# Performance work log

Measured on AMD Instinct MI355X. Metric: run time of the kernel, lower is better.

## Reference

```python
import math
import jax, jax.numpy as jnp
import numpy as np

B, N, D = 8, 2048, 256
NUM_ROLES = 3
ROLE_HUB, ROLE_MONITOR = 1, 2  # assumed ROLE_TO_ID mapping
NEG = -10000.0


def _lin_init(k, fan_in, shape):
    b = 1.0 / math.sqrt(fan_in)
    return jax.random.uniform(k, shape, jnp.float32, -b, b)


def setup_inputs() -> dict:
    key = jax.random.key(0)
    ks = jax.random.split(key, 20)
    inp = {
        'x': jax.random.normal(ks[0], (B, N, D), jnp.float32),
        'node_roles': jax.random.randint(ks[1], (B, N), 0, NUM_ROLES),
        'node_mask': jax.random.bernoulli(ks[2], 0.9, (B, N)),
        'ln_gamma': jnp.ones((D,), jnp.float32),
        'ln_beta': jnp.zeros((D,), jnp.float32),
        'role_emb': jax.random.normal(ks[3], (NUM_ROLES, D), jnp.float32),
    }
    names = ['q', 'k', 's', 'p', 'o']
    for i, nm in enumerate(names):
        inp['W' + nm] = _lin_init(ks[4 + 2 * i], D, (D, D))
        inp['b' + nm] = _lin_init(ks[5 + 2 * i], D, (D,))
    inp['Wg'] = _lin_init(ks[14], 2 * D, (2 * D, D))
    inp['bg'] = _lin_init(ks[15], 2 * D, (D,))
    return inp


def _layernorm(x, g, b):
    mu = jnp.mean(x, -1, keepdims=True)
    var = jnp.mean(jnp.square(x - mu), -1, keepdims=True)
    return (x - mu) * jax.lax.rsqrt(var + 1e-5) * g + b


def reference(x, node_roles, node_mask, ln_gamma, ln_beta, role_emb,
              Wq, bq, Wk, bk, Ws, bs, Wp, bp, Wo, bo, Wg, bg):
    normed = _layernorm(x, ln_gamma, ln_beta)
    role_bias = role_emb[node_roles]                      # [B,N,D]
    h = normed + role_bias
    query = h @ Wq + bq
    key_t = h @ Wk + bk
    sender = h @ Ws + bs
    payload = normed @ Wp + bp

    read_logits = jnp.einsum('bid,bjd->bij', query, key_t) / math.sqrt(D)
    fs = role_bias + sender
    forward_logits = jnp.einsum('bid,bjd->bij', fs, fs)
    logits = read_logits + 0.5 * forward_logits           # variant='selective'

    source_mask = node_mask                               # variant != 'memory_hubs'
    pair_mask = node_mask[:, :, None] & source_mask[:, None, :]
    eye = jnp.eye(N, dtype=bool)[None]
    pair_mask = pair_mask | (eye & node_mask[:, :, None] & node_mask[:, None, :])

    logits = jnp.where(pair_mask, logits, NEG)
    weights = jax.nn.softmax(logits, axis=-1)
    weights = jnp.where(pair_mask, weights, 0.0)

    message = jnp.einsum('bij,bjd->bid', weights, payload)
    gate = jax.nn.sigmoid(jnp.concatenate([x, message], axis=-1) @ Wg + bg)
    update = (gate * message) @ Wo + bo
    out = x + update                                      # dropout p=0

    entropy = -(weights * jnp.log(weights + 1e-8)).sum(-1).mean()
    # masked-mean replicates torch's weights[..., col_mask].mean() without dynamic shapes
    mon_cols = (node_roles == ROLE_MONITOR).any(0)        # [N]
    hub_cols = (node_roles == ROLE_HUB).any(0)
    def col_mean(cols):
        cnt = cols.sum() * B * N
        tot = (weights * cols[None, None, :].astype(weights.dtype)).sum()
        return jnp.where(cnt > 0, tot / jnp.maximum(cnt, 1), 0.0)
    return (out, entropy, col_mean(mon_cols), col_mean(hub_cols))
```

## Files before the change

### kernel.cpp

```cpp
#include <hip/hip_runtime.h>
#include <math.h>

#define BB 8
#define NN 2048
#define DD 256
#define MTOK 16384

typedef __bf16 bf16x8 __attribute__((ext_vector_type(8)));
typedef __bf16 bf16x4 __attribute__((ext_vector_type(4)));
typedef float f32x4 __attribute__((ext_vector_type(4)));

#define MFMA16(a, b, c) __builtin_amdgcn_mfma_f32_16x16x32_bf16(a, b, c, 0, 0, 0)

#define BARX()                              \
  do {                                      \
    asm volatile("" ::: "memory");          \
    __builtin_amdgcn_s_barrier();           \
    asm volatile("" ::: "memory");          \
  } while (0)
#define WAITVM(N)                                              \
  do {                                                         \
    asm volatile("s_waitcnt vmcnt(" #N ")" ::: "memory");      \
    __builtin_amdgcn_sched_barrier(0);                         \
  } while (0)

#define OFF_X16    0ull
#define OFF_N16    2097152ull
#define OFF_H16    4194304ull
#define OFF_GROW   8388608ull
#define OFF_GCOL   12582912ull
#define OFF_PTE    16777216ull
#define OFF_WT     19005440ull
#define OFF_STAT   19234816ull
#define OFF_ENT    23625728ull
#define OFF_MONR   23642112ull
#define OFF_HUBR   23658496ull
#define OFF_MONF   23674880ull
#define OFF_HUBF   23676928ull
#define OFF_MASK   23678976ull
#define OFF_PART   23683072ull
#define OFF_MSGN0  OFF_N16
#define OFF_MSGN1  OFF_H16
#define OFF_MSG16  OFF_PTE
#define OFF_GM16   OFF_GROW

__device__ __forceinline__ void gl_lds16(const void* g, void* l) {
  __builtin_amdgcn_global_load_lds(
      (const __attribute__((address_space(1))) unsigned int*)g,
      (__attribute__((address_space(3))) unsigned int*)l, 16, 0, 0);
}

__global__ __launch_bounds__(256) void setup_kernel(
    const float* __restrict__ x, const int* __restrict__ roles,
    const void* __restrict__ mraw,
    const float* __restrict__ gamma, const float* __restrict__ beta,
    const float* __restrict__ role_emb,
    const float* __restrict__ Wq, const float* __restrict__ Wk,
    const float* __restrict__ Ws, const float* __restrict__ Wp,
    const float* __restrict__ Wg, const float* __restrict__ Wo,
    __bf16* __restrict__ X16, __bf16* __restrict__ N16,
    __bf16* __restrict__ H16, __bf16* __restrict__ WT,
    unsigned char* __restrict__ mask8,
    float* __restrict__ monf, float* __restrict__ hubf) {
  __shared__ float T[64][65];
  int bid = blockIdx.x;
  int tid = threadIdx.x;
  if (bid < 4096) {
    int t = bid * 4 + (tid >> 6);
    int lane = tid & 63;
    size_t off = (size_t)t * DD + lane * 4;
    float4 xv = *(const float4*)(x + off);
    float s = xv.x + xv.y + xv.z + xv.w;
    float ss = xv.x * xv.x + xv.y * xv.y + xv.z * xv.z + xv.w * xv.w;
#pragma unroll
    for (int m = 1; m < 64; m <<= 1) {
      s += __shfl_xor(s, m, 64);
      ss += __shfl_xor(ss, m, 64);
    }
    float mu = s * (1.0f / 256.0f);
    float var = ss * (1.0f / 256.0f) - mu * mu;
    float inv = rsqrtf(var + 1e-5f);
    float4 g = *(const float4*)(gamma + lane * 4);
    float4 be = *(const float4*)(beta + lane * 4);
    float nv[4];
    nv[0] = (xv.x - mu) * inv * g.x + be.x;
    nv[1] = (xv.y - mu) * inv * g.y + be.y;
    nv[2] = (xv.z - mu) * inv * g.z + be.z;
    nv[3] = (xv.w - mu) * inv * g.w + be.w;
    int role = roles[t];
    float4 rb = *(const float4*)(role_emb + (size_t)role * DD + lane * 4);
    float rbv[4] = {rb.x, rb.y, rb.z, rb.w};
    bf16x4 xo, no, ho;
    float xf[4] = {xv.x, xv.y, xv.z, xv.w};
#pragma unroll
    for (int q = 0; q < 4; ++q) {
      xo[q] = (__bf16)xf[q];
      no[q] = (__bf16)nv[q];
      ho[q] = (__bf16)(nv[q] + rbv[q]);
    }
    *(bf16x4*)&X16[off] = xo;
    *(bf16x4*)&N16[off] = no;
    *(bf16x4*)&H16[off] = ho;
  } else if (bid < 4288) {
    int wblk = bid - 4096;
    int z = wblk >> 5, rem = wblk & 31;
    int bx = rem & 3, by = rem >> 2;
    const float* src;
    int K;
    size_t doff;
    switch (z) {
      case 0: src = Wq; K = 256; doff = 0; break;
      case 1: src = Wk; K = 256; doff = 65536; break;
      case 2: src = Ws; K = 256; doff = 131072; break;
      case 3: src = Wp; K = 256; doff = 196608; break;
      case 4: src = Wg; K = 512; doff = 262144; break;
      default: src = Wo; K = 256; doff = 393216; break;
    }
    int k0 = by * 64;
    if (k0 >= K) return;
    int n0 = bx * 64;
#pragma unroll
    for (int p = 0; p < 16; ++p) {
      int idx = p * 256 + tid;
      int r = idx >> 6, c = idx & 63;
      T[r][c] = src[(size_t)(k0 + r) * 256 + n0 + c];
    }
    __syncthreads();
#pragma unroll
    for (int p = 0; p < 16; ++p) {
      int idx = p * 256 + tid;
      int n = idx >> 6, k = idx & 63;
      WT[doff + (size_t)(n0 + n) * K + k0 + k] = (__bf16)T[k][n];
    }
  } else {
    int* csh = (int*)&T[0][0];
    if (tid == 0) { csh[0] = 0; csh[1] = 0; }
    __syncthreads();
    const unsigned char* raw = (const unsigned char*)mraw;
    int c0 = 0, c1 = 0;
    for (int i = tid; i < 4096; i += 256) {
      int nz = (raw[i] != 0) ? 1 : 0;
      if ((i & 3) == 0) c0 += nz; else c1 += nz;
    }
    atomicAdd(&csh[0], c0);
    atomicAdd(&csh[1], c1);
    __syncthreads();
    int k = (csh[0] == 0) ? 2 : ((csh[1] == 0) ? 0 : 1);
    int t = (bid - 4288) * 256 + tid;
    if (t < MTOK) {
      int v;
      if (k == 1)      v = (raw[t] != 0);
      else if (k == 0) v = (((const int*)mraw)[t] != 0);
      else             v = (((const float*)mraw)[t] != 0.0f);
      mask8[t] = (unsigned char)v;
    }
    if (t < NN) {
      int mon = 0, hub = 0;
#pragma unroll
      for (int b = 0; b < BB; ++b) {
        int r = roles[b * NN + t];
        mon |= (r == 2) ? 1 : 0;
        hub |= (r == 1) ? 1 : 0;
      }
      monf[t] = (float)mon;
      hubf[t] = (float)hub;
    }
  }
}

__global__ __launch_bounds__(256) void fill_pte_kernel(
    const int* __restrict__ roles, __bf16* __restrict__ PTE) {
  int idx = blockIdx.x * 256 + threadIdx.x;
  int b = idx >> 11, col = idx & 2047;
  int mon = 0, hub = 0;
#pragma unroll
  for (int bb = 0; bb < BB; ++bb) {
    int r = roles[bb * NN + col];
    mon |= (r == 2) ? 1 : 0;
    hub |= (r == 1) ? 1 : 0;
  }
  size_t rbase = ((size_t)(b * 272 + 256)) * 2048 + col;
  PTE[rbase] = (__bf16)(float)mon;
  PTE[rbase + 2048] = (__bf16)(float)hub;
  PTE[rbase + 2 * 2048] = (__bf16)1.0f;
#pragma unroll
  for (int r = 3; r < 16; ++r) PTE[rbase + (size_t)r * 2048] = (__bf16)0.0f;
}

__global__ __launch_bounds__(256, 3) void proj4_kernel(
    const __bf16* __restrict__ H16, const __bf16* __restrict__ N16,
    const __bf16* __restrict__ WT,
    const float* __restrict__ bq, const float* __restrict__ bk,
    const float* __restrict__ bs, const float* __restrict__ bp,
    const int* __restrict__ roles, const float* __restrict__ remb,
    __bf16* __restrict__ Grow, __bf16* __restrict__ Gcol,
    __bf16* __restrict__ PTE) {
  __shared__ __align__(16) unsigned char As[128 * 128];
  __shared__ __align__(16) unsigned char Bs[128 * 128];
  int z = blockIdx.z;
  const __bf16* A = (z == 3) ? N16 : H16;
  const __bf16* W = WT + (size_t)z * 65536;
  const float* bias = (z == 0) ? bq : (z == 1) ? bk : (z == 2) ? bs : bp;

  int tid = threadIdx.x;
  int w = tid >> 6, lane = tid & 63, ln15 = lane & 15, lq = lane >> 4;
  int wr = w >> 1, wc = w & 1;
  int row0 = blockIdx.y * 128, col0 = blockIdx.x * 128;
  f32x4 acc[4][4];
#pragma unroll
  for (int i = 0; i < 4; ++i)
#pragma unroll
    for (int j = 0; j < 4; ++j) acc[i][j] = (f32x4){0.f, 0.f, 0.f, 0.f};

  int lr = lane >> 3;
  int sb = ((lane & 7) * 16) ^ ((lr & 7) << 4);

  for (int kt = 0; kt < 4; ++kt) {
    __syncthreads();
#pragma unroll
    for (int i2 = 0; i2 < 4; ++i2) {
      int idx = w * 4 + i2;
      int grow = row0 + idx * 8 + lr;
      gl_lds16((const unsigned char*)A + (size_t)grow * 512 + kt * 128 + sb,
               As + idx * 1024);
    }
#pragma unroll
    for (int i2 = 0; i2 < 4; ++i2) {
      int idx = w * 4 + i2;
      int gcol = col0 + idx * 8 + lr;
      gl_lds16((const unsigned char*)W + (size_t)gcol * 512 + kt * 128 + sb,
               Bs + idx * 1024);
    }
    __syncthreads();
#pragma unroll
    for (int ks = 0; ks < 2; ++ks) {
      bf16x8 af[4], bfr[4];
#pragma unroll
      for (int i = 0; i < 4; ++i) {
        int rl = wr * 64 + i * 16 + ln15;
        int byteoff = (lq * 16 + ks * 64) ^ ((rl & 7) << 4);
        af[i] = *(const bf16x8*)(As + rl * 128 + byteoff);
      }
#pragma unroll
      for (int j = 0; j < 4; ++j) {
        int cl = wc * 64 + j * 16 + ln15;
        int byteoff = (lq * 16 + ks * 64) ^ ((cl & 7) << 4);
        bfr[j] = *(const bf16x8*)(Bs + cl * 128 + byteoff);
      }
#pragma unroll
      for (int i = 0; i < 4; ++i)
#pragma unroll
        for (int j = 0; j < 4; ++j) acc[i][j] = MFMA16(af[i], bfr[j], acc[i][j]);
    }
  }
  float bj[4];
#pragma unroll
  for (int j = 0; j < 4; ++j) bj[j] = bias[col0 + wc * 64 + j * 16 + ln15];
#pragma unroll
  for (int i = 0; i < 4; ++i) {
#pragma unroll
    for (int j = 0; j < 4; ++j) {
      int gcol = col0 + wc * 64 + j * 16 + ln15;
      int growb = row0 + wr * 64 + i * 16 + lq * 4;
      float o[4];
#pragma unroll
      for (int ri = 0; ri < 4; ++ri) o[ri] = acc[i][j][ri] + bj[j];
      if (z == 0) {
#pragma unroll
        for (int ri = 0; ri < 4; ++ri)
          Grow[(size_t)(growb + ri) * 512 + gcol] = (__bf16)(o[ri] * 0.0625f);
      } else if (z == 1) {
#pragma unroll
        for (int ri = 0; ri < 4; ++ri)
          Gcol[(size_t)(growb + ri) * 512 + gcol] = (__bf16)o[ri];
      } else if (z == 2) {
#pragma unroll
        for (int ri = 0; ri < 4; ++ri) {
          float oo = o[ri] + remb[(size_t)roles[growb + ri] * 256 + gcol];
          Grow[(size_t)(growb + ri) * 512 + 256 + gcol] =
              (__bf16)(oo * 0.70710678118f);
        }
      } else {
        bf16x4 v;
#pragma unroll
        for (int ri = 0; ri < 4; ++ri) v[ri] = (__bf16)o[ri];
        int b = growb >> 11, tok = growb & 2047;
        *(bf16x4*)&PTE[((size_t)(b * 272 + gcol)) * 2048 + tok] = v;
      }
    }
  }
}

__global__ __launch_bounds__(256, 2) void attn_kernel(
    const __bf16* __restrict__ Grow, const __bf16* __restrict__ Gcol,
    const __bf16* __restrict__ PTE, const unsigned char* __restrict__ mask8,
    __bf16* __restrict__ msgn0, __bf16* __restrict__ msgn1,
    float* __restrict__ statP) {
  __shared__ __align__(16) unsigned char GcLo[16384];
  __shared__ __align__(16) unsigned char GcHi[16384];
  __shared__ __align__(16) unsigned char PtS[2][17408];

  int tid = threadIdx.x;
  int w = tid >> 6, lane = tid & 63, ln15 = lane & 15, lq = lane >> 4;
  int id = blockIdx.x;
  int b = id & 7;
  int half = (id >> 3) & 1;
  int r0 = (id >> 4) * 64;
  size_t base = (size_t)b * NN;
  __bf16* msgn = half ? msgn1 : msgn0;
  float* statB = statP + (size_t)half * MTOK * 6;

  const unsigned char* gbaseK =
      (const unsigned char*)Gcol + (base + half * 1024) * 1024;
  const unsigned char* gbaseF =
      (const unsigned char*)Grow + (base + half * 1024) * 1024;
  const unsigned char* pbase =
      (const unsigned char*)PTE + (size_t)b * 272 * 4096 + half * 2048;

  bf16x8 Af[16];
  {
    const __bf16* gr = Grow + (base + r0 + w * 16 + ln15) * 512 + lq * 8;
#pragma unroll
    for (int kk = 0; kk < 16; ++kk) Af[kk] = *(const bf16x8*)(gr + kk * 32);
  }

  float m = -1e30f, T = 0.f;
  f32x4 macc[17];
#pragma unroll
  for (int nt = 0; nt < 17; ++nt) macc[nt] = (f32x4){0.f, 0.f, 0.f, 0.f};

  int pswz = (lq ^ ((ln15 >> 1) & 3)) << 4;
  int n0 = ((ln15 >> 2) * 8) + (ln15 & 3);
  int n1 = n0 + 4;
  int s0 = (((n0 & 3) | (((n0 >> 3) & 1) << 2))) << 4;
  int s1 = (((n1 & 3) | (((n1 >> 3) & 1) << 2))) << 4;
  int srcsw = ((lane & 3) ^ ((lane >> 3) & 3)) << 4;
  int glrow = lane >> 5;
  int glb = (lane & 31) * 16;

  auto STG = [&](const unsigned char* gb, int ch, unsigned char* dst, int koff) {
#pragma unroll
    for (int i = 0; i < 4; ++i) {
      int rp = w * 8 + 2 * i;
      int r = rp + glrow;
      int sbr = glb ^ ((((r & 3) | (((r >> 3) & 1) << 2))) << 4);
      gl_lds16(gb + (size_t)(ch * 32 + r) * 1024 + koff + sbr, dst + rp * 512);
    }
  };
  auto STPT = [&](int ch, int buf) {
#pragma unroll
    for (int i = 0; i < 4; ++i) {
      int idx = w * 4 + i;
      int drow = idx * 16 + (lane >> 2);
      gl_lds16(pbase + (size_t)drow * 4096 + ch * 64 + srcsw,
               &PtS[buf][idx * 1024]);
    }
    {
      int drow = 256 + (lane >> 2);
      gl_lds16(pbase + (size_t)drow * 4096 + ch * 64 + srcsw,
               &PtS[buf][16 * 1024]);
    }
  };

  STPT(0, 0);
  STG(gbaseK, 0, GcLo, 0);
  STG(gbaseF, 0, GcHi, 512);

  for (int ch = 0; ch < 32; ++ch) {
    int cur = ch & 1;
    WAITVM(4);
    BARX();
    STPT(ch + 1, cur ^ 1);

    f32x4 sa0 = (f32x4){0.f, 0.f, 0.f, 0.f};
    f32x4 sa1 = (f32x4){0.f, 0.f, 0.f, 0.f};
    __builtin_amdgcn_s_setprio(1);
#pragma unroll
    for (int kk = 0; kk < 8; ++kk) {
      bf16x8 bv0 = *(const bf16x8*)&GcLo[n0 * 512 + ((lq * 16 + kk * 64) ^ s0)];
      sa0 = MFMA16(bv0, Af[kk], sa0);
      bf16x8 bv1 = *(const bf16x8*)&GcLo[n1 * 512 + ((lq * 16 + kk * 64) ^ s1)];
      sa1 = MFMA16(bv1, Af[kk], sa1);
    }
    __builtin_amdgcn_s_setprio(0);

    WAITVM(5);
    BARX();
    STG(gbaseK, ch + 1, GcLo, 0);

    __builtin_amdgcn_s_setprio(1);
#pragma unroll
    for (int kk = 8; kk < 16; ++kk) {
      bf16x8 bv0 = *(const bf16x8*)&GcHi[n0 * 512 + ((lq * 16 + (kk - 8) * 64) ^ s0)];
      sa0 = MFMA16(bv0, Af[kk], sa0);
      bf16x8 bv1 = *(const bf16x8*)&GcHi[n1 * 512 + ((lq * 16 + (kk - 8) * 64) ^ s1)];
      sa1 = MFMA16(bv1, Af[kk], sa1);
    }
    __builtin_amdgcn_s_setprio(0);

    float sv[8] = {sa0[0], sa0[1], sa0[2], sa0[3], sa1[0], sa1[1], sa1[2], sa1[3]};
    unsigned long long mk = *(const unsigned long long*)(
        mask8 + base + half * 1024 + (size_t)ch * 32 + lq * 8);

    float mt = -1e30f;
#pragma unroll
    for (int i = 0; i < 8; ++i) {
      float li = ((mk >> (8 * i)) & 0xffull) ? sv[i] : -1e30f;
      mt = fmaxf(mt, li);
    }
    mt = fmaxf(mt, __shfl_xor(mt, 16));
    mt = fmaxf(mt, __shfl_xor(mt, 32));
    float mnew = fmaxf(m, mt);
    if (__any(mnew > m + 8.0f)) {
      float ci = __expf(m - mnew);
      float cir[4];
#pragma unroll
      for (int r = 0; r < 4; ++r)
        cir[r] = __shfl(ci, (lane & 48) + ((lane >> 2) & 12) + r);
#pragma unroll
      for (int nt = 0; nt < 17; ++nt) {
        macc[nt][0] *= cir[0]; macc[nt][1] *= cir[1];
        macc[nt][2] *= cir[2]; macc[nt][3] *= cir[3];
      }
      T *= ci;
      m = mnew;
    }
    float e[8], tl = 0.f;
#pragma unroll
    for (int i = 0; i < 8; ++i) {
      float ei = ((mk >> (8 * i)) & 0xffull) ? __expf(sv[i] - m) : 0.f;
      e[i] = ei;
      tl += ei * sv[i];
    }
    tl += __shfl_xor(tl, 16);
    tl += __shfl_xor(tl, 32);
    T += tl;
    bf16x8 ef;
#pragma unroll
    for (int i = 0; i < 8; ++i) ef[i] = (__bf16)e[i];

    __builtin_amdgcn_s_setprio(1);
#pragma unroll
    for (int nt = 0; nt < 17; ++nt) {
      int drow = nt * 16 + ln15;
      bf16x8 pv = *(const bf16x8*)&PtS[cur][drow * 64 + pswz];
      macc[nt] = MFMA16(ef, pv, macc[nt]);
    }
    __builtin_amdgcn_s_setprio(0);

    BARX();
    STG(gbaseF, ch + 1, GcHi, 512);
  }
  WAITVM(0);

#pragma unroll
  for (int r = 0; r < 4; ++r) {
    int grow = r0 + w * 16 + lq * 4 + r;
    size_t row = base + grow;
    float Z = __shfl(macc[16][r], (lane & 48) + 2);
    float invZ = (Z > 0.f) ? (1.0f / Z) : 0.f;
#pragma unroll
    for (int nt = 0; nt < 16; ++nt)
      msgn[row * 256 + nt * 16 + ln15] = (__bf16)(macc[nt][r] * invZ);
    float Tm = __shfl(macc[16][r], (lane & 48) + 0);
    float Th = __shfl(macc[16][r], (lane & 48) + 1);
    float Tr = __shfl(T, (lane & 48) + ((lane >> 2) & 12) + r);
    float mr = __shfl(m, (lane & 48) + ((lane >> 2) & 12) + r);
    if (ln15 == 0) {
      float* stt = statB + row * 6;
      stt[0] = mr; stt[1] = Tr; stt[2] = Z; stt[3] = Tm; stt[4] = Th;
    }
  }
}

__global__ __launch_bounds__(256) void merge_kernel(
    const __bf16* __restrict__ msgn0, const __bf16* __restrict__ msgn1,
    const float* __restrict__ statP, const unsigned char* __restrict__ mask8,
    __bf16* __restrict__ MSG16, float* __restrict__ entr,
    float* __restrict__ monr, float* __restrict__ hubr) {
  int row = blockIdx.x * 4 + (threadIdx.x >> 6);
  int lane = threadIdx.x & 63;
  const float* s0 = statP + (size_t)row * 6;
  const float* s1 = statP + (size_t)(MTOK + row) * 6;
  float m0 = s0[0], T0 = s0[1], Z0 = s0[2], Tm0 = s0[3], Th0 = s0[4];
  float m1 = s1[0], T1 = s1[1], Z1 = s1[2], Tm1 = s1[3], Th1 = s1[4];
  int valid = mask8[row] != 0;
  float mm = fmaxf(m0, m1);
  float c0 = __expf(m0 - mm), c1 = __expf(m1 - mm);
  float w0 = c0 * Z0, w1 = c1 * Z1;
  float Z = w0 + w1;
  int ok = valid && (Z > 0.f);
  float invZ = ok ? (1.0f / Z) : 0.0f;
  float rw0 = w0 * invZ, rw1 = w1 * invZ;
  bf16x4 p0 = *(const bf16x4*)(msgn0 + (size_t)row * 256 + lane * 4);
  bf16x4 p1 = *(const bf16x4*)(msgn1 + (size_t)row * 256 + lane * 4);
  bf16x4 o;
#pragma unroll
  for (int q = 0; q < 4; ++q)
    o[q] = (__bf16)(rw0 * (float)p0[q] + rw1 * (float)p1[q]);
  *(bf16x4*)&MSG16[(size_t)row * 256 + lane * 4] = o;
  if (lane == 0) {
    float T = c0 * T0 + c1 * T1;
    float Tm = c0 * Tm0 + c1 * Tm1;
    float Th = c0 * Th0 + c1 * Th1;
    entr[row] = ok ? (__logf(Z) + mm - T * invZ) : 0.0f;
    monr[row] = ok ? (Tm * invZ) : 0.0f;
    hubr[row] = ok ? (Th * invZ) : 0.0f;
  }
}

template <int K, int MODE>
__global__ __launch_bounds__(256) void gemmb_kernel(
    const __bf16* __restrict__ A0, const __bf16* __restrict__ A1,
    const __bf16* __restrict__ WT, const float* __restrict__ bias,
    const float* __restrict__ xf, const __bf16* __restrict__ msg16,
    void* __restrict__ dst0) {
  __shared__ __align__(16) unsigned char As[128 * 128];
  __shared__ __align__(16) unsigned char Bs[64 * 128];
  int tid = threadIdx.x;
  int w = tid >> 6, lane = tid & 63, ln15 = lane & 15, lq = lane >> 4;
  int wr = w >> 1, wc = w & 1;
  int row0 = blockIdx.y * 128, col0 = blockIdx.x * 64;
  f32x4 acc[4][2];
#pragma unroll
  for (int i = 0; i < 4; ++i)
#pragma unroll
    for (int j = 0; j < 2; ++j) acc[i][j] = (f32x4){0.f, 0.f, 0.f, 0.f};

  int lr = lane >> 3;
  int sb = ((lane & 7) * 16) ^ ((lr & 7) << 4);

  for (int kt = 0; kt < K / 64; ++kt) {
    const __bf16* Ab = A0;
    int ktl = kt;
    if (K == 512 && kt >= 4) { Ab = A1; ktl = kt - 4; }
    __syncthreads();
#pragma unroll
    for (int i2 = 0; i2 < 4; ++i2) {
      int idx = w * 4 + i2;
      int grow = row0 + idx * 8 + lr;
      gl_lds16((const unsigned char*)Ab + (size_t)grow * 512 + ktl * 128 + sb,
               As + idx * 1024);
    }
#pragma unroll
    for (int i2 = 0; i2 < 2; ++i2) {
      int idx = w * 2 + i2;
      int gcol = col0 + idx * 8 + lr;
      gl_lds16((const unsigned char*)WT + (size_t)gcol * (K * 2) + kt * 128 + sb,
               Bs + idx * 1024);
    }
    __syncthreads();
#pragma unroll
    for (int ks = 0; ks < 2; ++ks) {
      bf16x8 af[4], bfr[2];
#pragma unroll
      for (int i = 0; i < 4; ++i) {
        int rl = wr * 64 + i * 16 + ln15;
        int byteoff = (lq * 16 + ks * 64) ^ ((rl & 7) << 4);
        af[i] = *(const bf16x8*)(As + rl * 128 + byteoff);
      }
#pragma unroll
      for (int j = 0; j < 2; ++j) {
        int cl = wc * 32 + j * 16 + ln15;
        int byteoff = (lq * 16 + ks * 64) ^ ((cl & 7) << 4);
        bfr[j] = *(const bf16x8*)(Bs + cl * 128 + byteoff);
      }
#pragma unroll
      for (int i = 0; i < 4; ++i)
#pragma unroll
        for (int j = 0; j < 2; ++j) acc[i][j] = MFMA16(af[i], bfr[j], acc[i][j]);
    }
  }
  float bj[2];
#pragma unroll
  for (int j = 0; j < 2; ++j) bj[j] = bias[col0 + wc * 32 + j * 16 + ln15];
#pragma unroll
  for (int i = 0; i < 4; ++i) {
#pragma unroll
    for (int ri = 0; ri < 4; ++ri) {
      int grow = row0 + wr * 64 + i * 16 + lq * 4 + ri;
#pragma unroll
      for (int j = 0; j < 2; ++j) {
        int gcol = col0 + wc * 32 + j * 16 + ln15;
        float o = acc[i][j][ri] + bj[j];
        if (MODE == 4) {
          float sg = 1.0f / (1.0f + __expf(-o));
          float mv = (float)msg16[(size_t)grow * 256 + gcol];
          ((__bf16*)dst0)[(size_t)grow * 256 + gcol] = (__bf16)(sg * mv);
        } else {
          ((float*)dst0)[(size_t)grow * 256 + gcol] =
              o + xf[(size_t)grow * 256 + gcol];
        }
      }
    }
  }
}

__device__ __forceinline__ float block_sum(float v, float* sh) {
  __syncthreads();
  sh[threadIdx.x] = v;
  __syncthreads();
  for (int s = 128; s > 0; s >>= 1) {
    if ((int)threadIdx.x < s) sh[threadIdx.x] += sh[threadIdx.x + s];
    __syncthreads();
  }
  return sh[0];
}

__global__ __launch_bounds__(256) void reduce1_kernel(
    const float* __restrict__ entr, const float* __restrict__ monr,
    const float* __restrict__ hubr, float* __restrict__ partial) {
  __shared__ float sh[256];
  int t = blockIdx.x * 256 + threadIdx.x;
  float es = entr[t], ms = monr[t], hs = hubr[t];
  float e = block_sum(es, sh);
  float mo = block_sum(ms, sh);
  float hu = block_sum(hs, sh);
  if (threadIdx.x == 0) {
    partial[blockIdx.x * 4 + 0] = e;
    partial[blockIdx.x * 4 + 1] = mo;
    partial[blockIdx.x * 4 + 2] = hu;
  }
}

__global__ __launch_bounds__(256) void reduce2_kernel(
    const float* __restrict__ partial, const float* __restrict__ monf,
    const float* __restrict__ hubf, float* __restrict__ out3) {
  __shared__ float sh[256];
  float es = 0.f, ms = 0.f, hs = 0.f, cmf = 0.f, chf = 0.f;
  if (threadIdx.x < 64) {
    es = partial[threadIdx.x * 4 + 0];
    ms = partial[threadIdx.x * 4 + 1];
    hs = partial[threadIdx.x * 4 + 2];
  }
  for (int j = threadIdx.x; j < NN; j += 256) { cmf += monf[j]; chf += hubf[j]; }
  float esum = block_sum(es, sh);
  float msum = block_sum(ms, sh);
  float hsum = block_sum(hs, sh);
  float cmsum = block_sum(cmf, sh);
  float chsum = block_sum(chf, sh);
  if (threadIdx.x == 0) {
    out3[0] = esum / 16384.0f;
    out3[1] = (cmsum > 0.f) ? (msum / (cmsum * 16384.0f)) : 0.0f;
    out3[2] = (chsum > 0.f) ? (hsum / (chsum * 16384.0f)) : 0.0f;
  }
}

extern "C" void kernel_launch(void* const* d_in, const int* in_sizes, int n_in,
                              void* d_out, int out_size, void* d_ws, size_t ws_size,
                              hipStream_t stream) {
  const float* x = (const float*)d_in[0];
  const int* roles = (const int*)d_in[1];
  const void* mraw = d_in[2];
  const float* gamma = (const float*)d_in[3];
  const float* beta = (const float*)d_in[4];
  const float* remb = (const float*)d_in[5];
  const float* Wq = (const float*)d_in[6];
  const float* bq = (const float*)d_in[7];
  const float* Wk = (const float*)d_in[8];
  const float* bk = (const float*)d_in[9];
  const float* Ws = (const float*)d_in[10];
  const float* bs = (const float*)d_in[11];
  const float* Wp = (const float*)d_in[12];
  const float* bp = (const float*)d_in[13];
  const float* Wo = (const float*)d_in[14];
  const float* bo = (const float*)d_in[15];
  const float* Wg = (const float*)d_in[16];
  const float* bg = (const float*)d_in[17];

  float* ws = (float*)d_ws;
  __bf16* X16 = (__bf16*)(ws + OFF_X16);
  __bf16* N16 = (__bf16*)(ws + OFF_N16);
  __bf16* H16 = (__bf16*)(ws + OFF_H16);
  __bf16* Grow = (__bf16*)(ws + OFF_GROW);
  __bf16* Gcol = (__bf16*)(ws + OFF_GCOL);
  __bf16* PTE = (__bf16*)(ws + OFF_PTE);
  __bf16* WT = (__bf16*)(ws + OFF_WT);
  float* statP = ws + OFF_STAT;
  __bf16* msgn0 = (__bf16*)(ws + OFF_MSGN0);
  __bf16* msgn1 = (__bf16*)(ws + OFF_MSGN1);
  float* partial = ws + OFF_PART;
  __bf16* MSG16 = (__bf16*)(ws + OFF_MSG16);
  __bf16* GM16 = (__bf16*)(ws + OFF_GM16);
  float* entr = ws + OFF_ENT;
  float* monr = ws + OFF_MONR;
  float* hubr = ws + OFF_HUBR;
  float* monfp = ws + OFF_MONF;
  float* hubfp = ws + OFF_HUBF;
  unsigned char* mask8 = (unsigned char*)(ws + OFF_MASK);
  float* out = (float*)d_out;

  __bf16* WTg = WT + 262144;
  __bf16* WTo = WT + 393216;

  setup_kernel<<<4352, 256, 0, stream>>>(x, roles, mraw, gamma, beta, remb,
                                         Wq, Wk, Ws, Wp, Wg, Wo,
                                         X16, N16, H16, WT, mask8, monfp, hubfp);
  fill_pte_kernel<<<64, 256, 0, stream>>>(roles, PTE);
  proj4_kernel<<<dim3(2, 128, 4), 256, 0, stream>>>(
      H16, N16, WT, bq, bk, bs, bp, roles, remb, Grow, Gcol, PTE);
  attn_kernel<<<512, 256, 0, stream>>>(Grow, Gcol, PTE, mask8, msgn0, msgn1,
                                       statP);
  merge_kernel<<<4096, 256, 0, stream>>>(msgn0, msgn1, statP, mask8, MSG16,
                                         entr, monr, hubr);
  dim3 gg(4, 128);
  gemmb_kernel<512, 4><<<gg, 256, 0, stream>>>(X16, MSG16, WTg, bg, nullptr,
                                               MSG16, GM16);
  gemmb_kernel<256, 5><<<gg, 256, 0, stream>>>(GM16, nullptr, WTo, bo, x,
                                               nullptr, out);
  reduce1_kernel<<<64, 256, 0, stream>>>(entr, monr, hubr, partial);
  reduce2_kernel<<<1, 256, 0, stream>>>(partial, monfp, hubfp, out + 4194304);
}
```

Measured before the change: 165.7 us.

## Split attention key range into thirds and single-buffer payload tile for occupancy

Result: slower. 287.2 us (+73.3%).

```diff
diff --git a/kernel.cpp b/kernel.cpp
--- a/kernel.cpp
+++ b/kernel.cpp
@@ -27,6 +27,7 @@
 #define OFF_X16    0ull
 #define OFF_N16    2097152ull
 #define OFF_H16    4194304ull
+#define OFF_MSGN2t 6291456ull
 #define OFF_GROW   8388608ull
 #define OFF_GCOL   12582912ull
 #define OFF_PTE    16777216ull
@@ -43,6 +44,9 @@
 #define OFF_MSGN1  OFF_H16
 #define OFF_MSG16  OFF_PTE
 #define OFF_GM16   OFF_GROW
+
+__device__ __constant__ int kKvOff[3] = {0, 704, 1376};
+__device__ __constant__ int kNch[3] = {22, 21, 21};
 
 __device__ __forceinline__ void gl_lds16(const void* g, void* l) {
   __builtin_amdgcn_global_load_lds(
@@ -291,31 +295,33 @@
   }
 }
 
-__global__ __launch_bounds__(256, 2) void attn_kernel(
+__global__ __launch_bounds__(256, 3) void attn_kernel(
     const __bf16* __restrict__ Grow, const __bf16* __restrict__ Gcol,
     const __bf16* __restrict__ PTE, const unsigned char* __restrict__ mask8,
     __bf16* __restrict__ msgn0, __bf16* __restrict__ msgn1,
-    float* __restrict__ statP) {
+    __bf16* __restrict__ msgn2, float* __restrict__ statP) {
   __shared__ __align__(16) unsigned char GcLo[16384];
   __shared__ __align__(16) unsigned char GcHi[16384];
-  __shared__ __align__(16) unsigned char PtS[2][17408];
+  __shared__ __align__(16) unsigned char PtS[17408];
 
   int tid = threadIdx.x;
   int w = tid >> 6, lane = tid & 63, ln15 = lane & 15, lq = lane >> 4;
   int id = blockIdx.x;
   int b = id & 7;
-  int half = (id >> 3) & 1;
-  int r0 = (id >> 4) * 64;
+  int third = (id >> 3) % 3;
+  int r0 = (id / 24) * 64;
   size_t base = (size_t)b * NN;
-  __bf16* msgn = half ? msgn1 : msgn0;
-  float* statB = statP + (size_t)half * MTOK * 6;
+  int kvoff = kKvOff[third];
+  int nch = kNch[third];
+  __bf16* msgn = (third == 0) ? msgn0 : (third == 1) ? msgn1 : msgn2;
+  float* statB = statP + (size_t)third * MTOK * 6;
 
   const unsigned char* gbaseK =
-      (const unsigned char*)Gcol + (base + half * 1024) * 1024;
+      (const unsigned char*)Gcol + (base + kvoff) * 1024;
   const unsigned char* gbaseF =
-      (const unsigned char*)Grow + (base + half * 1024) * 1024;
+      (const unsigned char*)Grow + (base + kvoff) * 1024;
   const unsigned char* pbase =
-      (const unsigned char*)PTE + (size_t)b * 272 * 4096 + half * 2048;
+      (const unsigned char*)PTE + (size_t)b * 272 * 4096 + (size_t)kvoff * 2;
 
   bf16x8 Af[16];
   {
@@ -347,30 +353,28 @@
       gl_lds16(gb + (size_t)(ch * 32 + r) * 1024 + koff + sbr, dst + rp * 512);
     }
   };
-  auto STPT = [&](int ch, int buf) {
+  auto STPT = [&](int ch) {
 #pragma unroll
     for (int i = 0; i < 4; ++i) {
       int idx = w * 4 + i;
       int drow = idx * 16 + (lane >> 2);
       gl_lds16(pbase + (size_t)drow * 4096 + ch * 64 + srcsw,
-               &PtS[buf][idx * 1024]);
+               PtS + idx * 1024);
     }
     {
       int drow = 256 + (lane >> 2);
       gl_lds16(pbase + (size_t)drow * 4096 + ch * 64 + srcsw,
-               &PtS[buf][16 * 1024]);
+               PtS + 16 * 1024);
     }
   };
 
-  STPT(0, 0);
   STG(gbaseK, 0, GcLo, 0);
   STG(gbaseF, 0, GcHi, 512);
-
-  for (int ch = 0; ch < 32; ++ch) {
-    int cur = ch & 1;
-    WAITVM(4);
+  STPT(0);
+
+  for (int ch = 0; ch < nch; ++ch) {
+    WAITVM(9);
     BARX();
-    STPT(ch + 1, cur ^ 1);
 
     f32x4 sa0 = (f32x4){0.f, 0.f, 0.f, 0.f};
     f32x4 sa1 = (f32x4){0.f, 0.f, 0.f, 0.f};
@@ -400,7 +404,7 @@
 
     float sv[8] = {sa0[0], sa0[1], sa0[2], sa0[3], sa1[0], sa1[1], sa1[2], sa1[3]};
     unsigned long long mk = *(const unsigned long long*)(
-        mask8 + base + half * 1024 + (size_t)ch * 32 + lq * 8);
+        mask8 + base + kvoff + (size_t)ch * 32 + lq * 8);
 
     float mt = -1e30f;
 #pragma unroll
@@ -439,17 +443,21 @@
 #pragma unroll
     for (int i = 0; i < 8; ++i) ef[i] = (__bf16)e[i];
 
+    WAITVM(4);
+    BARX();
+    STG(gbaseF, ch + 1, GcHi, 512);
+
     __builtin_amdgcn_s_setprio(1);
 #pragma unroll
     for (int nt = 0; nt < 17; ++nt) {
       int drow = nt * 16 + ln15;
-      bf16x8 pv = *(const bf16x8*)&PtS[cur][drow * 64 + pswz];
+      bf16x8 pv = *(const bf16x8*)&PtS[drow * 64 + pswz];
       macc[nt] = MFMA16(ef, pv, macc[nt]);
     }
     __builtin_amdgcn_s_setprio(0);
 
     BARX();
-    STG(gbaseF, ch + 1, GcHi, 512);
+    STPT(ch + 1);
   }
   WAITVM(0);
 
@@ -475,34 +483,41 @@
 
 __global__ __launch_bounds__(256) void merge_kernel(
     const __bf16* __restrict__ msgn0, const __bf16* __restrict__ msgn1,
-    const float* __restrict__ statP, const unsigned char* __restrict__ mask8,
+    const __bf16* __restrict__ msgn2, const float* __restrict__ statP,
+    const unsigned char* __restrict__ mask8,
     __bf16* __restrict__ MSG16, float* __restrict__ entr,
     float* __restrict__ monr, float* __restrict__ hubr) {
   int row = blockIdx.x * 4 + (threadIdx.x >> 6);
   int lane = threadIdx.x & 63;
-  const float* s0 = statP + (size_t)row * 6;
-  const float* s1 = statP + (size_t)(MTOK + row) * 6;
-  float m0 = s0[0], T0 = s0[1], Z0 = s0[2], Tm0 = s0[3], Th0 = s0[4];
-  float m1 = s1[0], T1 = s1[1], Z1 = s1[2], Tm1 = s1[3], Th1 = s1[4];
-  int valid = mask8[row] != 0;
-  float mm = fmaxf(m0, m1);
-  float c0 = __expf(m0 - mm), c1 = __expf(m1 - mm);
-  float w0 = c0 * Z0, w1 = c1 * Z1;
-  float Z = w0 + w1;
-  int ok = valid && (Z > 0.f);
+  float mq[3], Tq[3], Zq[3], Tmq[3], Thq[3];
+#pragma unroll
+  for (int q = 0; q < 3; ++q) {
+    const float* s = statP + (size_t)q * MTOK * 6 + (size_t)row * 6;
+    mq[q] = s[0]; Tq[q] = s[1]; Zq[q] = s[2]; Tmq[q] = s[3]; Thq[q] = s[4];
+  }
+  float mm = fmaxf(fmaxf(mq[0], mq[1]), mq[2]);
+  float cq[3], wq[3], Z = 0.f;
+#pragma unroll
+  for (int q = 0; q < 3; ++q) {
+    cq[q] = __expf(mq[q] - mm);
+    wq[q] = cq[q] * Zq[q];
+    Z += wq[q];
+  }
+  int ok = (mask8[row] != 0) && (Z > 0.f);
   float invZ = ok ? (1.0f / Z) : 0.0f;
-  float rw0 = w0 * invZ, rw1 = w1 * invZ;
   bf16x4 p0 = *(const bf16x4*)(msgn0 + (size_t)row * 256 + lane * 4);
   bf16x4 p1 = *(const bf16x4*)(msgn1 + (size_t)row * 256 + lane * 4);
+  bf16x4 p2 = *(const bf16x4*)(msgn2 + (size_t)row * 256 + lane * 4);
+  float r0 = wq[0] * invZ, r1 = wq[1] * invZ, r2 = wq[2] * invZ;
   bf16x4 o;
 #pragma unroll
   for (int q = 0; q < 4; ++q)
-    o[q] = (__bf16)(rw0 * (float)p0[q] + rw1 * (float)p1[q]);
+    o[q] = (__bf16)(r0 * (float)p0[q] + r1 * (float)p1[q] + r2 * (float)p2[q]);
   *(bf16x4*)&MSG16[(size_t)row * 256 + lane * 4] = o;
   if (lane == 0) {
-    float T = c0 * T0 + c1 * T1;
-    float Tm = c0 * Tm0 + c1 * Tm1;
-    float Th = c0 * Th0 + c1 * Th1;
+    float T = cq[0] * Tq[0] + cq[1] * Tq[1] + cq[2] * Tq[2];
+    float Tm = cq[0] * Tmq[0] + cq[1] * Tmq[1] + cq[2] * Tmq[2];
+    float Th = cq[0] * Thq[0] + cq[1] * Thq[1] + cq[2] * Thq[2];
     entr[row] = ok ? (__logf(Z) + mm - T * invZ) : 0.0f;
     monr[row] = ok ? (Tm * invZ) : 0.0f;
     hubr[row] = ok ? (Th * invZ) : 0.0f;
@@ -679,6 +694,7 @@
   float* statP = ws + OFF_STAT;
   __bf16* msgn0 = (__bf16*)(ws + OFF_MSGN0);
   __bf16* msgn1 = (__bf16*)(ws + OFF_MSGN1);
+  __bf16* msgn2 = (__bf16*)(ws + OFF_MSGN2t);
   float* partial = ws + OFF_PART;
   __bf16* MSG16 = (__bf16*)(ws + OFF_MSG16);
   __bf16* GM16 = (__bf16*)(ws + OFF_GM16);
@@ -699,10 +715,10 @@
   fill_pte_kernel<<<64, 256, 0, stream>>>(roles, PTE);
   proj4_kernel<<<dim3(2, 128, 4), 256, 0, stream>>>(
       H16, N16, WT, bq, bk, bs, bp, roles, remb, Grow, Gcol, PTE);
-  attn_kernel<<<512, 256, 0, stream>>>(Grow, Gcol, PTE, mask8, msgn0, msgn1,
-                                       statP);
-  merge_kernel<<<4096, 256, 0, stream>>>(msgn0, msgn1, statP, mask8, MSG16,
-                                         entr, monr, hubr);
+  attn_kernel<<<768, 256, 0, stream>>>(Grow, Gcol, PTE, mask8,
+                                       msgn0, msgn1, msgn2, statP);
+  merge_kernel<<<4096, 256, 0, stream>>>(msgn0, msgn1, msgn2, statP, mask8,
+                                         MSG16, entr, monr, hubr);
   dim3 gg(4, 128);
   gemmb_kernel<512, 4><<<gg, 256, 0, stream>>>(X16, MSG16, WTg, bg, nullptr,
                                                MSG16, GM16);
```
